# Optimization experiments

Measured on AMD Instinct MI355X. Metric: run time of the kernel, lower is better.

## Reference

```python
import jax, jax.numpy as jnp
import numpy as np

TOP_K = 2

def setup_inputs() -> dict:
    key = jax.random.key(0)
    k1, k2 = jax.random.split(key)
    D, E = 4096, 64
    hidden_states = jax.random.normal(k1, (2, 8192, D), dtype=jnp.float32)
    W = jax.random.normal(k2, (E, D), dtype=jnp.float32) / np.sqrt(D)
    b = jnp.zeros((E,), dtype=jnp.float32)
    return {"hidden_states": hidden_states, "W": W, "b": b}

def reference(hidden_states, W, b):
    # gate: logits [B, S, E]
    logits = jnp.einsum('bsd,ed->bse', hidden_states, W) + b
    scores = jax.nn.softmax(logits, axis=-1)
    top_k_values, top_k_indices = jax.lax.top_k(scores, TOP_K)
    return ((top_k_indices, top_k_values), scores)
```

## Files before the change

### kernel.cpp

```cpp
#include <hip/hip_runtime.h>
#include <math.h>

#define D_DIM 4096
#define E_DIM 64
#define TM 64
#define KSPLIT 4
#define KPART (D_DIM / KSPLIT)
#define CHK 64
#define NCH (KPART / CHK)
#define WROW 72

typedef __attribute__((ext_vector_type(8))) short bf16x8;
typedef __attribute__((ext_vector_type(4))) float f32x4;

__device__ inline void split3(const f32x4 a0, const f32x4 a1,
                              bf16x8& fh, bf16x8& fm, bf16x8& fl) {
    uint uh[8], um[8], ul[8];
    float f[8] = {a0[0], a0[1], a0[2], a0[3], a1[0], a1[1], a1[2], a1[3]};
    #pragma unroll
    for (int j = 0; j < 8; ++j) {
        const uint u = __float_as_uint(f[j]);
        const uint h = u & 0xFFFF0000u;
        const float r = f[j] - __uint_as_float(h);
        const uint m = __float_as_uint(r) & 0xFFFF0000u;
        const float r2 = r - __uint_as_float(m);
        uh[j] = h; um[j] = m; ul[j] = __float_as_uint(r2);
    }
    union { bf16x8 v; uint u[4]; } H, M, L;
    #pragma unroll
    for (int j = 0; j < 4; ++j) {
        H.u[j] = (uh[2*j] >> 16) | (uh[2*j+1] & 0xFFFF0000u);
        M.u[j] = (um[2*j] >> 16) | (um[2*j+1] & 0xFFFF0000u);
        L.u[j] = (ul[2*j] >> 16) | (ul[2*j+1] & 0xFFFF0000u);
    }
    fh = H.v; fm = M.v; fl = L.v;
}

__global__ __launch_bounds__(256, 4) void router_gemm(
    const float* __restrict__ hs,
    const float* __restrict__ W,
    float* __restrict__ logits,
    int nTok)
{
    __shared__ short wsh[E_DIM * WROW];
    __shared__ short wsm[E_DIM * WROW];
    __shared__ short wsl[E_DIM * WROW];

    const int tid  = threadIdx.x;
    const int lane = tid & 63;
    const int wv   = tid >> 6;
    const int part = blockIdx.x & (KSPLIT - 1);
    const int tb   = (blockIdx.x >> 2) * TM;
    const int kb   = part * KPART;

    const int l15 = lane & 15;
    const int lq  = lane >> 4;

    const float* aptr = hs + (size_t)(tb + wv * 16 + l15) * D_DIM + kb + lq * 8;
    const int we = tid >> 2;
    const int wq = tid & 3;
    const float* wptr = W + (size_t)we * D_DIM + kb + wq * 16;

    f32x4 acc[4];
    #pragma unroll
    for (int t = 0; t < 4; ++t) acc[t] = (f32x4){0.f, 0.f, 0.f, 0.f};

    f32x4 ca[4], pa[4], wr[4];

    auto loadA = [&](int ch, f32x4* dst) {
        const float* p = aptr + ch * CHK;
        dst[0] = *(const f32x4*)(p);
        dst[1] = *(const f32x4*)(p + 4);
        dst[2] = *(const f32x4*)(p + 32);
        dst[3] = *(const f32x4*)(p + 36);
    };
    auto loadW = [&](int ch) {
        const float* p = wptr + ch * CHK;
        wr[0] = *(const f32x4*)(p);
        wr[1] = *(const f32x4*)(p + 4);
        wr[2] = *(const f32x4*)(p + 8);
        wr[3] = *(const f32x4*)(p + 12);
    };
    auto storeW = [&]() {
        bf16x8 h0, m0, l0, h1, m1, l1;
        split3(wr[0], wr[1], h0, m0, l0);
        split3(wr[2], wr[3], h1, m1, l1);
        const int base = we * WROW + wq * 16;
        *(bf16x8*)&wsh[base] = h0;  *(bf16x8*)&wsh[base + 8] = h1;
        *(bf16x8*)&wsm[base] = m0;  *(bf16x8*)&wsm[base + 8] = m1;
        *(bf16x8*)&wsl[base] = l0;  *(bf16x8*)&wsl[base + 8] = l1;
    };
    auto compute = [&](const f32x4* a) {
        #pragma unroll
        for (int s = 0; s < 2; ++s) {
            bf16x8 ah, am, al;
            split3(a[2 * s], a[2 * s + 1], ah, am, al);
            const int koff = s * 32 + lq * 8;
            #pragma unroll
            for (int t = 0; t < 4; ++t) {
                const int rb = (t * 16 + l15) * WROW + koff;
                const bf16x8 bh = *(const bf16x8*)&wsh[rb];
                const bf16x8 bm = *(const bf16x8*)&wsm[rb];
                const bf16x8 bl = *(const bf16x8*)&wsl[rb];
                acc[t] = __builtin_amdgcn_mfma_f32_16x16x32_bf16(ah, bh, acc[t], 0, 0, 0);
                acc[t] = __builtin_amdgcn_mfma_f32_16x16x32_bf16(ah, bm, acc[t], 0, 0, 0);
                acc[t] = __builtin_amdgcn_mfma_f32_16x16x32_bf16(am, bh, acc[t], 0, 0, 0);
                acc[t] = __builtin_amdgcn_mfma_f32_16x16x32_bf16(ah, bl, acc[t], 0, 0, 0);
                acc[t] = __builtin_amdgcn_mfma_f32_16x16x32_bf16(al, bh, acc[t], 0, 0, 0);
                acc[t] = __builtin_amdgcn_mfma_f32_16x16x32_bf16(am, bm, acc[t], 0, 0, 0);
            }
        }
    };

    loadA(0, ca);
    loadW(0);
    storeW();
    __syncthreads();
    #pragma unroll 1
    for (int ch = 0; ch < NCH; ++ch) {
        const bool last = (ch == NCH - 1);
        if (!last) loadA(ch + 1, pa);
        compute(ca);
        if (!last) {
            loadW(ch + 1);
            __syncthreads();
            storeW();
            __syncthreads();
            #pragma unroll
            for (int i = 0; i < 4; ++i) ca[i] = pa[i];
        }
    }

    float* dst = logits + (size_t)(tb + wv * 16) * E_DIM;
    #pragma unroll
    for (int t = 0; t < 4; ++t)
        #pragma unroll
        for (int r = 0; r < 4; ++r)
            unsafeAtomicAdd(&dst[(size_t)(lq * 4 + r) * E_DIM + t * 16 + l15], acc[t][r]);
}

__global__ __launch_bounds__(256, 4) void router_epilogue(
    const float* __restrict__ bias,
    float* __restrict__ out,
    int nTok)
{
    const int tid = threadIdx.x;
    const int tok = blockIdx.x * 64 + (tid >> 2);
    const int g   = tid & 3;

    float* out_idx = out;
    float* out_val = out + (size_t)nTok * 2;
    float* sc      = out + (size_t)nTok * 4;

    float* src = sc + (size_t)tok * E_DIM + g * 16;
    float v[16];
    #pragma unroll
    for (int j = 0; j < 4; ++j) {
        const f32x4 x = *(const f32x4*)(src + j * 4);
        const f32x4 b = *(const f32x4*)(bias + g * 16 + j * 4);
        v[j * 4 + 0] = x[0] + b[0];
        v[j * 4 + 1] = x[1] + b[1];
        v[j * 4 + 2] = x[2] + b[2];
        v[j * 4 + 3] = x[3] + b[3];
    }

    float b1 = -INFINITY, b2 = -INFINITY;
    int i1 = 0, i2 = 0;
    #pragma unroll
    for (int j = 0; j < 16; ++j) {
        const float x = v[j];
        const int idx = g * 16 + j;
        if (x > b1)      { b2 = b1; i2 = i1; b1 = x; i1 = idx; }
        else if (x > b2) { b2 = x; i2 = idx; }
    }
    #pragma unroll
    for (int d = 1; d <= 2; d <<= 1) {
        const float ob1 = __shfl_xor(b1, d);
        const int   oi1 = __shfl_xor(i1, d);
        const float ob2 = __shfl_xor(b2, d);
        const int   oi2 = __shfl_xor(i2, d);
        if (ob1 > b1 || (ob1 == b1 && oi1 < i1)) {
            if (b1 > ob2 || (b1 == ob2 && i1 < oi2)) { b2 = b1; i2 = i1; }
            else                                     { b2 = ob2; i2 = oi2; }
            b1 = ob1; i1 = oi1;
        } else {
            if (ob1 > b2 || (ob1 == b2 && oi1 < i2)) { b2 = ob1; i2 = oi1; }
        }
    }
    const float m = b1;

    float e[16];
    float s = 0.f;
    #pragma unroll
    for (int j = 0; j < 16; ++j) { e[j] = __expf(v[j] - m); s += e[j]; }
    s += __shfl_xor(s, 1);
    s += __shfl_xor(s, 2);
    const float inv = 1.f / s;

    if (g == 0) {
        out_idx[(size_t)tok * 2 + 0] = (float)i1;
        out_idx[(size_t)tok * 2 + 1] = (float)i2;
        out_val[(size_t)tok * 2 + 0] = inv;
        out_val[(size_t)tok * 2 + 1] = __expf(b2 - m) * inv;
    }

    #pragma unroll
    for (int j = 0; j < 4; ++j) {
        f32x4 o;
        o[0] = e[j * 4 + 0] * inv;
        o[1] = e[j * 4 + 1] * inv;
        o[2] = e[j * 4 + 2] * inv;
        o[3] = e[j * 4 + 3] * inv;
        *(f32x4*)(src + j * 4) = o;
    }
}

extern "C" void kernel_launch(void* const* d_in, const int* in_sizes, int n_in,
                              void* d_out, int out_size, void* d_ws, size_t ws_size,
                              hipStream_t stream) {
    const float* hs = (const float*)d_in[0];
    const float* W  = (const float*)d_in[1];
    const float* b  = (const float*)d_in[2];
    float* out = (float*)d_out;
    const int nTok = in_sizes[0] / D_DIM;

    float* logits = out + (size_t)nTok * 4;
    hipMemsetAsync(logits, 0, (size_t)nTok * E_DIM * sizeof(float), stream);

    dim3 g1(nTok / TM * KSPLIT), b1(256);
    router_gemm<<<g1, b1, 0, stream>>>(hs, W, logits, nTok);

    dim3 g2(nTok / 64), b2(256);
    router_epilogue<<<g2, b2, 0, stream>>>(b, out, nTok);
}
```

Baseline: 385.1 us.

## Pre-split W into bf16 planes and fuse GEMM with softmax/top-k epilogue

Adds a presplit kernel that converts W once per call into three bf16 planes in workspace, so the main kernel reads B fragments straight from global or L2 instead of splitting and staging them in LDS with barriers. The K-split now runs across the four waves of a block and is reduced through shared memory rather than global atomics. The bias, softmax and top-2 epilogue is fused into the same kernel, which removes the memset and the logits round-trip through HBM. In exchange, each block handles only 32 tokens, B fragments come from uncoalesced global loads, and the kernel uses about 41KB of LDS, which may limit occupancy.

```diff
diff --git a/kernel.cpp b/kernel.cpp
--- a/kernel.cpp
+++ b/kernel.cpp
@@ -3,15 +3,37 @@
 
 #define D_DIM 4096
 #define E_DIM 64
-#define TM 64
-#define KSPLIT 4
-#define KPART (D_DIM / KSPLIT)
+#define TM 32
 #define CHK 64
-#define NCH (KPART / CHK)
-#define WROW 72
+#define KQ 1024
+#define NCH (KQ / CHK)
 
 typedef __attribute__((ext_vector_type(8))) short bf16x8;
+typedef __attribute__((ext_vector_type(4))) short s16x4;
 typedef __attribute__((ext_vector_type(4))) float f32x4;
+
+__global__ __launch_bounds__(256) void presplit(
+    const float* __restrict__ W,
+    short* __restrict__ wh, short* __restrict__ wm, short* __restrict__ wl)
+{
+    const int i = (blockIdx.x * 256 + threadIdx.x) * 4;
+    const f32x4 v = *(const f32x4*)&W[i];
+    s16x4 h, m, l;
+    #pragma unroll
+    for (int j = 0; j < 4; ++j) {
+        const uint u  = __float_as_uint(v[j]);
+        const uint hh = u & 0xFFFF0000u;
+        const float r  = v[j] - __uint_as_float(hh);
+        const uint mm = __float_as_uint(r) & 0xFFFF0000u;
+        const float r2 = r - __uint_as_float(mm);
+        h[j] = (short)(hh >> 16);
+        m[j] = (short)(mm >> 16);
+        l[j] = (short)(__float_as_uint(r2) >> 16);
+    }
+    *(s16x4*)&wh[i] = h;
+    *(s16x4*)&wm[i] = m;
+    *(s16x4*)&wl[i] = l;
+}
 
 __device__ inline void split3(const f32x4 a0, const f32x4 a1,
                               bf16x8& fh, bf16x8& fm, bf16x8& fl) {
@@ -36,182 +58,182 @@
     fh = H.v; fm = M.v; fl = L.v;
 }
 
-__global__ __launch_bounds__(256, 4) void router_gemm(
+__global__ __launch_bounds__(256) void router_main(
     const float* __restrict__ hs,
-    const float* __restrict__ W,
-    float* __restrict__ logits,
-    int nTok)
-{
-    __shared__ short wsh[E_DIM * WROW];
-    __shared__ short wsm[E_DIM * WROW];
-    __shared__ short wsl[E_DIM * WROW];
-
-    const int tid  = threadIdx.x;
-    const int lane = tid & 63;
-    const int wv   = tid >> 6;
-    const int part = blockIdx.x & (KSPLIT - 1);
-    const int tb   = (blockIdx.x >> 2) * TM;
-    const int kb   = part * KPART;
-
-    const int l15 = lane & 15;
-    const int lq  = lane >> 4;
-
-    const float* aptr = hs + (size_t)(tb + wv * 16 + l15) * D_DIM + kb + lq * 8;
-    const int we = tid >> 2;
-    const int wq = tid & 3;
-    const float* wptr = W + (size_t)we * D_DIM + kb + wq * 16;
-
-    f32x4 acc[4];
-    #pragma unroll
-    for (int t = 0; t < 4; ++t) acc[t] = (f32x4){0.f, 0.f, 0.f, 0.f};
-
-    f32x4 ca[4], pa[4], wr[4];
-
-    auto loadA = [&](int ch, f32x4* dst) {
-        const float* p = aptr + ch * CHK;
-        dst[0] = *(const f32x4*)(p);
-        dst[1] = *(const f32x4*)(p + 4);
-        dst[2] = *(const f32x4*)(p + 32);
-        dst[3] = *(const f32x4*)(p + 36);
-    };
-    auto loadW = [&](int ch) {
-        const float* p = wptr + ch * CHK;
-        wr[0] = *(const f32x4*)(p);
-        wr[1] = *(const f32x4*)(p + 4);
-        wr[2] = *(const f32x4*)(p + 8);
-        wr[3] = *(const f32x4*)(p + 12);
-    };
-    auto storeW = [&]() {
-        bf16x8 h0, m0, l0, h1, m1, l1;
-        split3(wr[0], wr[1], h0, m0, l0);
-        split3(wr[2], wr[3], h1, m1, l1);
-        const int base = we * WROW + wq * 16;
-        *(bf16x8*)&wsh[base] = h0;  *(bf16x8*)&wsh[base + 8] = h1;
-        *(bf16x8*)&wsm[base] = m0;  *(bf16x8*)&wsm[base + 8] = m1;
-        *(bf16x8*)&wsl[base] = l0;  *(bf16x8*)&wsl[base + 8] = l1;
-    };
-    auto compute = [&](const f32x4* a) {
-        #pragma unroll
-        for (int s = 0; s < 2; ++s) {
-            bf16x8 ah, am, al;
-            split3(a[2 * s], a[2 * s + 1], ah, am, al);
-            const int koff = s * 32 + lq * 8;
-            #pragma unroll
-            for (int t = 0; t < 4; ++t) {
-                const int rb = (t * 16 + l15) * WROW + koff;
-                const bf16x8 bh = *(const bf16x8*)&wsh[rb];
-                const bf16x8 bm = *(const bf16x8*)&wsm[rb];
-                const bf16x8 bl = *(const bf16x8*)&wsl[rb];
-                acc[t] = __builtin_amdgcn_mfma_f32_16x16x32_bf16(ah, bh, acc[t], 0, 0, 0);
-                acc[t] = __builtin_amdgcn_mfma_f32_16x16x32_bf16(ah, bm, acc[t], 0, 0, 0);
-                acc[t] = __builtin_amdgcn_mfma_f32_16x16x32_bf16(am, bh, acc[t], 0, 0, 0);
-                acc[t] = __builtin_amdgcn_mfma_f32_16x16x32_bf16(ah, bl, acc[t], 0, 0, 0);
-                acc[t] = __builtin_amdgcn_mfma_f32_16x16x32_bf16(al, bh, acc[t], 0, 0, 0);
-                acc[t] = __builtin_amdgcn_mfma_f32_16x16x32_bf16(am, bm, acc[t], 0, 0, 0);
-            }
-        }
-    };
-
-    loadA(0, ca);
-    loadW(0);
-    storeW();
-    __syncthreads();
-    #pragma unroll 1
-    for (int ch = 0; ch < NCH; ++ch) {
-        const bool last = (ch == NCH - 1);
-        if (!last) loadA(ch + 1, pa);
-        compute(ca);
-        if (!last) {
-            loadW(ch + 1);
-            __syncthreads();
-            storeW();
-            __syncthreads();
-            #pragma unroll
-            for (int i = 0; i < 4; ++i) ca[i] = pa[i];
-        }
-    }
-
-    float* dst = logits + (size_t)(tb + wv * 16) * E_DIM;
-    #pragma unroll
-    for (int t = 0; t < 4; ++t)
-        #pragma unroll
-        for (int r = 0; r < 4; ++r)
-            unsafeAtomicAdd(&dst[(size_t)(lq * 4 + r) * E_DIM + t * 16 + l15], acc[t][r]);
-}
-
-__global__ __launch_bounds__(256, 4) void router_epilogue(
+    const short* __restrict__ wh,
+    const short* __restrict__ wm,
+    const short* __restrict__ wl,
     const float* __restrict__ bias,
     float* __restrict__ out,
     int nTok)
 {
-    const int tid = threadIdx.x;
-    const int tok = blockIdx.x * 64 + (tid >> 2);
-    const int g   = tid & 3;
+    __shared__ float red[4][TM][E_DIM];
+    __shared__ float fin[TM * E_DIM];
+    __shared__ float s_m[TM], s_inv[TM];
+
+    const int tid  = threadIdx.x;
+    const int lane = tid & 63;
+    const int w    = tid >> 6;
+    const int tb   = blockIdx.x * TM;
+    const int l15  = lane & 15;
+    const int lq   = lane >> 4;
+    const int kb   = w * KQ;
+
+    const float* a0 = hs + (size_t)(tb + l15) * D_DIM + kb + lq * 8;
+    const float* a1 = a0 + (size_t)16 * D_DIM;
+
+    f32x4 acc[2][4];
+    #pragma unroll
+    for (int m = 0; m < 2; ++m)
+        #pragma unroll
+        for (int t = 0; t < 4; ++t)
+            acc[m][t] = (f32x4){0.f, 0.f, 0.f, 0.f};
+
+    f32x4 ca[2][4], pa[2][4];
+
+    auto loadA = [&](int ch, f32x4 (*dst)[4]) {
+        #pragma unroll
+        for (int m = 0; m < 2; ++m) {
+            const float* p = (m ? a1 : a0) + ch * CHK;
+            dst[m][0] = *(const f32x4*)(p);
+            dst[m][1] = *(const f32x4*)(p + 4);
+            dst[m][2] = *(const f32x4*)(p + 32);
+            dst[m][3] = *(const f32x4*)(p + 36);
+        }
+    };
+
+    auto compute = [&](int ch, f32x4 (*a)[4]) {
+        const size_t kk = (size_t)kb + ch * CHK;
+        #pragma unroll
+        for (int s = 0; s < 2; ++s) {
+            bf16x8 ah0, am0, al0, ah1, am1, al1;
+            split3(a[0][2*s], a[0][2*s+1], ah0, am0, al0);
+            split3(a[1][2*s], a[1][2*s+1], ah1, am1, al1);
+            #pragma unroll
+            for (int t = 0; t < 4; ++t) {
+                const size_t wb = (size_t)(t * 16 + l15) * D_DIM + kk + s * 32 + lq * 8;
+                const bf16x8 bh = *(const bf16x8*)&wh[wb];
+                const bf16x8 bm = *(const bf16x8*)&wm[wb];
+                const bf16x8 bl = *(const bf16x8*)&wl[wb];
+                acc[0][t] = __builtin_amdgcn_mfma_f32_16x16x32_bf16(ah0, bh, acc[0][t], 0, 0, 0);
+                acc[0][t] = __builtin_amdgcn_mfma_f32_16x16x32_bf16(ah0, bm, acc[0][t], 0, 0, 0);
+                acc[0][t] = __builtin_amdgcn_mfma_f32_16x16x32_bf16(am0, bh, acc[0][t], 0, 0, 0);
+                acc[0][t] = __builtin_amdgcn_mfma_f32_16x16x32_bf16(ah0, bl, acc[0][t], 0, 0, 0);
+                acc[0][t] = __builtin_amdgcn_mfma_f32_16x16x32_bf16(al0, bh, acc[0][t], 0, 0, 0);
+                acc[0][t] = __builtin_amdgcn_mfma_f32_16x16x32_bf16(am0, bm, acc[0][t], 0, 0, 0);
+                acc[1][t] = __builtin_amdgcn_mfma_f32_16x16x32_bf16(ah1, bh, acc[1][t], 0, 0, 0);
+                acc[1][t] = __builtin_amdgcn_mfma_f32_16x16x32_bf16(ah1, bm, acc[1][t], 0, 0, 0);
+                acc[1][t] = __builtin_amdgcn_mfma_f32_16x16x32_bf16(am1, bh, acc[1][t], 0, 0, 0);
+                acc[1][t] = __builtin_amdgcn_mfma_f32_16x16x32_bf16(ah1, bl, acc[1][t], 0, 0, 0);
+                acc[1][t] = __builtin_amdgcn_mfma_f32_16x16x32_bf16(al1, bh, acc[1][t], 0, 0, 0);
+                acc[1][t] = __builtin_amdgcn_mfma_f32_16x16x32_bf16(am1, bm, acc[1][t], 0, 0, 0);
+            }
+        }
+    };
+
+    loadA(0, ca);
+    #pragma unroll 1
+    for (int ch = 0; ch < NCH; ch += 2) {
+        loadA(ch + 1, pa);
+        compute(ch, ca);
+        if (ch + 2 < NCH) loadA(ch + 2, ca);
+        compute(ch + 1, pa);
+    }
+
+    #pragma unroll
+    for (int m = 0; m < 2; ++m)
+        #pragma unroll
+        for (int t = 0; t < 4; ++t)
+            #pragma unroll
+            for (int r = 0; r < 4; ++r)
+                red[w][m * 16 + lq * 4 + r][t * 16 + l15] = acc[m][t][r];
+    __syncthreads();
+
+    {
+        const int f = tid * 8;
+        const float* rp = &red[0][0][0];
+        f32x4 v0 = *(const f32x4*)&rp[f];
+        f32x4 v1 = *(const f32x4*)&rp[f + 4];
+        #pragma unroll
+        for (int ww = 1; ww < 4; ++ww) {
+            const f32x4 u0 = *(const f32x4*)&rp[ww * (TM * E_DIM) + f];
+            const f32x4 u1 = *(const f32x4*)&rp[ww * (TM * E_DIM) + f + 4];
+            v0 += u0; v1 += u1;
+        }
+        const int e0 = f & 63;
+        v0 += *(const f32x4*)&bias[e0];
+        v1 += *(const f32x4*)&bias[e0 + 4];
+        *(f32x4*)&fin[f]     = v0;
+        *(f32x4*)&fin[f + 4] = v1;
+    }
+    __syncthreads();
 
     float* out_idx = out;
     float* out_val = out + (size_t)nTok * 2;
     float* sc      = out + (size_t)nTok * 4;
 
-    float* src = sc + (size_t)tok * E_DIM + g * 16;
-    float v[16];
-    #pragma unroll
-    for (int j = 0; j < 4; ++j) {
-        const f32x4 x = *(const f32x4*)(src + j * 4);
-        const f32x4 b = *(const f32x4*)(bias + g * 16 + j * 4);
-        v[j * 4 + 0] = x[0] + b[0];
-        v[j * 4 + 1] = x[1] + b[1];
-        v[j * 4 + 2] = x[2] + b[2];
-        v[j * 4 + 3] = x[3] + b[3];
-    }
-
-    float b1 = -INFINITY, b2 = -INFINITY;
-    int i1 = 0, i2 = 0;
-    #pragma unroll
-    for (int j = 0; j < 16; ++j) {
-        const float x = v[j];
-        const int idx = g * 16 + j;
-        if (x > b1)      { b2 = b1; i2 = i1; b1 = x; i1 = idx; }
-        else if (x > b2) { b2 = x; i2 = idx; }
-    }
-    #pragma unroll
-    for (int d = 1; d <= 2; d <<= 1) {
-        const float ob1 = __shfl_xor(b1, d);
-        const int   oi1 = __shfl_xor(i1, d);
-        const float ob2 = __shfl_xor(b2, d);
-        const int   oi2 = __shfl_xor(i2, d);
-        if (ob1 > b1 || (ob1 == b1 && oi1 < i1)) {
-            if (b1 > ob2 || (b1 == ob2 && i1 < oi2)) { b2 = b1; i2 = i1; }
-            else                                     { b2 = ob2; i2 = oi2; }
-            b1 = ob1; i1 = oi1;
-        } else {
-            if (ob1 > b2 || (ob1 == b2 && oi1 < i2)) { b2 = ob1; i2 = oi1; }
-        }
-    }
-    const float m = b1;
-
-    float e[16];
-    float s = 0.f;
-    #pragma unroll
-    for (int j = 0; j < 16; ++j) { e[j] = __expf(v[j] - m); s += e[j]; }
-    s += __shfl_xor(s, 1);
-    s += __shfl_xor(s, 2);
-    const float inv = 1.f / s;
-
-    if (g == 0) {
-        out_idx[(size_t)tok * 2 + 0] = (float)i1;
-        out_idx[(size_t)tok * 2 + 1] = (float)i2;
-        out_val[(size_t)tok * 2 + 0] = inv;
-        out_val[(size_t)tok * 2 + 1] = __expf(b2 - m) * inv;
-    }
-
-    #pragma unroll
-    for (int j = 0; j < 4; ++j) {
-        f32x4 o;
-        o[0] = e[j * 4 + 0] * inv;
-        o[1] = e[j * 4 + 1] * inv;
-        o[2] = e[j * 4 + 2] * inv;
-        o[3] = e[j * 4 + 3] * inv;
-        *(f32x4*)(src + j * 4) = o;
+    if (tid < TM * 4) {
+        const int tok = tid >> 2;
+        const int g   = tid & 3;
+        float v[16];
+        #pragma unroll
+        for (int j = 0; j < 4; ++j) {
+            const f32x4 x = *(const f32x4*)&fin[tok * E_DIM + g * 16 + j * 4];
+            v[j*4+0] = x[0]; v[j*4+1] = x[1]; v[j*4+2] = x[2]; v[j*4+3] = x[3];
+        }
+        float b1 = -INFINITY, b2 = -INFINITY;
+        int i1 = 0, i2 = 0;
+        #pragma unroll
+        for (int j = 0; j < 16; ++j) {
+            const float x = v[j];
+            const int idx = g * 16 + j;
+            if (x > b1)      { b2 = b1; i2 = i1; b1 = x; i1 = idx; }
+            else if (x > b2) { b2 = x; i2 = idx; }
+        }
+        #pragma unroll
+        for (int d = 1; d <= 2; d <<= 1) {
+            const float ob1 = __shfl_xor(b1, d);
+            const int   oi1 = __shfl_xor(i1, d);
+            const float ob2 = __shfl_xor(b2, d);
+            const int   oi2 = __shfl_xor(i2, d);
+            if (ob1 > b1 || (ob1 == b1 && oi1 < i1)) {
+                if (b1 > ob2 || (b1 == ob2 && i1 < oi2)) { b2 = b1; i2 = i1; }
+                else                                     { b2 = ob2; i2 = oi2; }
+                b1 = ob1; i1 = oi1;
+            } else {
+                if (ob1 > b2 || (ob1 == b2 && oi1 < i2)) { b2 = ob1; i2 = oi1; }
+            }
+        }
+        const float m = b1;
+        float s = 0.f;
+        #pragma unroll
+        for (int j = 0; j < 16; ++j) s += __expf(v[j] - m);
+        s += __shfl_xor(s, 1);
+        s += __shfl_xor(s, 2);
+        const float inv = 1.f / s;
+        if (g == 0) {
+            const size_t gt = (size_t)(tb + tok);
+            out_idx[gt * 2 + 0] = (float)i1;
+            out_idx[gt * 2 + 1] = (float)i2;
+            out_val[gt * 2 + 0] = inv;
+            out_val[gt * 2 + 1] = __expf(b2 - m) * inv;
+            s_m[tok] = m;
+            s_inv[tok] = inv;
+        }
+    }
+    __syncthreads();
+
+    {
+        const int f   = tid * 8;
+        const int tok = f >> 6;
+        const float m = s_m[tok], inv = s_inv[tok];
+        f32x4 o0, o1;
+        #pragma unroll
+        for (int j = 0; j < 4; ++j) o0[j] = __expf(fin[f + j] - m) * inv;
+        #pragma unroll
+        for (int j = 0; j < 4; ++j) o1[j] = __expf(fin[f + 4 + j] - m) * inv;
+        *(f32x4*)&sc[(size_t)tb * E_DIM + f]     = o0;
+        *(f32x4*)&sc[(size_t)tb * E_DIM + f + 4] = o1;
     }
 }
 
@@ -224,12 +246,11 @@
     float* out = (float*)d_out;
     const int nTok = in_sizes[0] / D_DIM;
 
-    float* logits = out + (size_t)nTok * 4;
-    hipMemsetAsync(logits, 0, (size_t)nTok * E_DIM * sizeof(float), stream);
-
-    dim3 g1(nTok / TM * KSPLIT), b1(256);
-    router_gemm<<<g1, b1, 0, stream>>>(hs, W, logits, nTok);
-
-    dim3 g2(nTok / 64), b2(256);
-    router_epilogue<<<g2, b2, 0, stream>>>(b, out, nTok);
-}
+    short* wsp = (short*)d_ws;
+    short* wh = wsp;
+    short* wm = wsp + E_DIM * D_DIM;
+    short* wl = wsp + 2 * E_DIM * D_DIM;
+
+    presplit<<<dim3(E_DIM * D_DIM / 1024), dim3(256), 0, stream>>>(W, wh, wm, wl);
+    router_main<<<dim3(nTok / TM), dim3(256), 0, stream>>>(hs, wh, wm, wl, b, out, nTok);
+}
```

New measurement: 424.9 us. +10.3%, slower.
